# Optimization experiments

Hardware: AMD Instinct MI355X
Metric: run time of the kernel (lower is better)

## Reference

```python
import jax, jax.numpy as jnp
import numpy as np

H = 64          # hidden_size
L = 5           # num_layers
D_IN = 45       # input_size
D_LAT = 128     # latent dim
D_OUT = 4       # output classes


def _lstm_layer(x, W_ih, W_hh, b):
    """One LSTM layer, batch_first input x:[B,T,D]. PyTorch gate order i,f,g,o."""
    # Precompute input contribution for all timesteps: [B,T,4H]
    xg = jnp.einsum('btd,gd->btg', x, W_ih) + b
    xg = jnp.swapaxes(xg, 0, 1)  # [T,B,4H] for scan
    B = x.shape[0]
    h0 = jnp.zeros((B, H), x.dtype)
    c0 = jnp.zeros((B, H), x.dtype)

    def step(carry, xt):
        h, c = carry
        g = xt + h @ W_hh.T                      # [B,4H]
        i, f, gg, o = jnp.split(g, 4, axis=-1)
        c = jax.nn.sigmoid(f) * c + jax.nn.sigmoid(i) * jnp.tanh(gg)
        h = jax.nn.sigmoid(o) * jnp.tanh(c)
        return (h, c), h

    (_, _), hs = jax.lax.scan(step, (h0, c0), xg)  # hs: [T,B,H]
    return jnp.swapaxes(hs, 0, 1)                  # [B,T,H]


def setup_inputs() -> dict:
    key = jax.random.key(0)
    ks = jax.random.split(key, 12)
    s = 1.0 / np.sqrt(H)  # PyTorch LSTM init scale
    x = jax.random.normal(ks[0], (256, 2048, D_IN), jnp.float32)
    W_ih0 = jax.random.uniform(ks[1], (4 * H, D_IN), jnp.float32, -s, s)
    W_ih_rest = jax.random.uniform(ks[2], (L - 1, 4 * H, H), jnp.float32, -s, s)
    W_hh = jax.random.uniform(ks[3], (L, 4 * H, H), jnp.float32, -s, s)
    b_ih = jax.random.uniform(ks[4], (L, 4 * H), jnp.float32, -s, s)
    b_hh = jax.random.uniform(ks[5], (L, 4 * H), jnp.float32, -s, s)
    Wl = jax.random.normal(ks[6], (D_LAT, H), jnp.float32) * 0.05
    bl = jnp.zeros((D_LAT,), jnp.float32)
    Wo = jax.random.normal(ks[7], (D_OUT, D_LAT), jnp.float32) * 0.05
    bo = jnp.zeros((D_OUT,), jnp.float32)
    return dict(x=x, W_ih0=W_ih0, W_ih_rest=W_ih_rest, W_hh=W_hh,
                b_ih=b_ih, b_hh=b_hh, Wl=Wl, bl=bl, Wo=Wo, bo=bo)


def reference(x, W_ih0, W_ih_rest, W_hh, b_ih, b_hh, Wl, bl, Wo, bo):
    # 5-layer LSTM (eval mode: inter-layer dropout inactive)
    h = _lstm_layer(x, W_ih0, W_hh[0], b_ih[0] + b_hh[0])
    for l in range(1, L):
        h = _lstm_layer(h, W_ih_rest[l - 1], W_hh[l], b_ih[l] + b_hh[l])
    last = h[:, -1, :]                                  # [B,H]
    features = jax.nn.gelu(last @ Wl.T + bl, approximate=False)  # [B,128]
    out = jax.nn.relu(features @ Wo.T + bo)             # [B,4]
    return out, features
```

## Files before the change

### kernel.cpp

```cpp
#include <hip/hip_runtime.h>
#include <hip/hip_fp16.h>
#include <math.h>

#define NCH   1024
#define KMAX  1034
#define HID   64
typedef unsigned int uint;
typedef __attribute__((ext_vector_type(2))) _Float16 h2t;

__device__ __forceinline__ float sigmoid_(float x){ return 1.0f/(1.0f+__expf(-x)); }
__device__ __forceinline__ float tanh_(float x){ float e=__expf(2.0f*x); return 1.0f-2.0f/(e+1.0f); }

__device__ __forceinline__ float fdot2_(uint w, uint h, float acc){
#if __has_builtin(__builtin_amdgcn_fdot2)
    return __builtin_amdgcn_fdot2(__builtin_bit_cast(h2t,w), __builtin_bit_cast(h2t,h), acc, false);
#else
    __half2 wv = *reinterpret_cast<const __half2*>(&w);
    __half2 hv = *reinterpret_cast<const __half2*>(&h);
    float2 wf = __half22float2(wv), hf = __half22float2(hv);
    return fmaf(wf.x, hf.x, fmaf(wf.y, hf.y, acc));
#endif
}
__device__ __forceinline__ uint packh(float a, float b){
    uint ha = (uint)__half_as_ushort(__float2half(a));
    uint hb = (uint)__half_as_ushort(__float2half(b));
    return (hb<<16)|ha;
}
__device__ __forceinline__ uint4 pack8(const float* p){
    return make_uint4(packh(p[0],p[1]), packh(p[2],p[3]), packh(p[4],p[5]), packh(p[6],p[7]));
}

#define DOT4(A, W, H) do{ \
    A=fdot2_((W).x,(H).x,A); A=fdot2_((W).y,(H).y,A); \
    A=fdot2_((W).z,(H).z,A); A=fdot2_((W).w,(H).w,A); }while(0)

__global__ __attribute__((amdgpu_waves_per_eu(1,1))) __launch_bounds__(256)
void lstm_pipe4(const float* __restrict__ x,
                const float* __restrict__ W_ih0,
                const float* __restrict__ W_ih_rest,
                const float* __restrict__ W_hh,
                const float* __restrict__ b_ih,
                const float* __restrict__ b_hh,
                float* __restrict__ h_last)
{
    __shared__ float s_xg[2][5][2][256];
    __shared__ uint  s_wo [5][8][64][4];
    __shared__ uint  s_wih[10][8][64][4];
    __shared__ uint  s_hh[4][2][2][32];
    __shared__ uint  s_h16[5][32];
    __shared__ uint  s_x[2][2][24];

    const int tid  = threadIdx.x;
    const int wave = tid >> 6;
    const int lane = tid & 63;
    const int sm   = blockIdx.x;
    const float* x_s = x + (size_t)sm * 2048 * 45;
    float* hlast_g = h_last + (size_t)sm * HID;

    uint4 wU[48];
    float b0=0,b1=0,b2=0,b3=0,b4=0,b5=0,b6=0,b7=0,b8=0,b9=0;
    float cA=0.f, cB=0.f;

    if (wave == 0 || wave == 1){
#pragma unroll
        for (int li=0; li<2; ++li){
            const int L = wave*2 + li;
            const float* base = W_hh + (size_t)L*256*64;
#pragma unroll
            for (int d=0; d<8; ++d){
                wU[li*24 + 0*8 + d] = pack8(base + (size_t)(  0+lane)*64 + 8*d);
                wU[li*24 + 1*8 + d] = pack8(base + (size_t)( 64+lane)*64 + 8*d);
                wU[li*24 + 2*8 + d] = pack8(base + (size_t)(128+lane)*64 + 8*d);
                *(uint4*)&s_wo[L][d][lane][0] = pack8(base + (size_t)(192+lane)*64 + 8*d);
            }
            if (lane<32) s_h16[L][lane]=0u;
        }
#pragma unroll
        for (int g=0; g<2; ++g){
            const int row = wave*128 + g*64 + lane;
            const float* src = W_ih_rest + ((size_t)3*256 + row)*64;
            const int grp = 6 + wave*2 + g;
#pragma unroll
            for (int d=0; d<8; ++d)
                *(uint4*)&s_wih[grp][d][lane][0] = pack8(src + 8*d);
        }
        { int r0 = 4*256 + wave*128 + lane, r1 = r0 + 64;
          b0 = b_ih[r0]+b_hh[r0]; b1 = b_ih[r1]+b_hh[r1]; }
    } else if (wave == 2){
        const float* base = W_hh + (size_t)4*256*64;
#pragma unroll
        for (int d=0; d<8; ++d){
            wU[0*8+d] = pack8(base + (size_t)(  0+lane)*64 + 8*d);
            wU[1*8+d] = pack8(base + (size_t)( 64+lane)*64 + 8*d);
            wU[2*8+d] = pack8(base + (size_t)(128+lane)*64 + 8*d);
            *(uint4*)&s_wo[4][d][lane][0] = pack8(base + (size_t)(192+lane)*64 + 8*d);
        }
        if (lane<32) s_h16[4][lane]=0u;
#pragma unroll
        for (int g=0; g<4; ++g){
            const float* src = W_ih0 + (size_t)(g*64+lane)*45;
#pragma unroll
            for (int d=0; d<6; ++d){
                float e0=(8*d+0<45)?src[8*d+0]:0.f, e1=(8*d+1<45)?src[8*d+1]:0.f;
                float e2=(8*d+2<45)?src[8*d+2]:0.f, e3=(8*d+3<45)?src[8*d+3]:0.f;
                float e4=(8*d+4<45)?src[8*d+4]:0.f, e5=(8*d+5<45)?src[8*d+5]:0.f;
                float e6=(8*d+6<45)?src[8*d+6]:0.f, e7=(8*d+7<45)?src[8*d+7]:0.f;
                wU[24 + g*6 + d] = make_uint4(packh(e0,e1),packh(e2,e3),packh(e4,e5),packh(e6,e7));
            }
        }
        { int r;
          r=      lane; b0=b_ih[r]+b_hh[r];
          r=  64+lane;  b1=b_ih[r]+b_hh[r];
          r= 128+lane;  b2=b_ih[r]+b_hh[r];
          r= 192+lane;  b3=b_ih[r]+b_hh[r]; }
#pragma unroll
        for (int g=0; g<2; ++g){
            const int row = 128 + g*64 + lane;
            const float* src = W_ih_rest + ((size_t)1*256 + row)*64;
#pragma unroll
            for (int d=0; d<8; ++d)
                *(uint4*)&s_wih[g][d][lane][0] = pack8(src + 8*d);
        }
        { int r0=2*256+128+lane, r1=2*256+192+lane;
          b4=b_ih[r0]+b_hh[r0]; b5=b_ih[r1]+b_hh[r1]; }
        if (lane < 12){
            int bb=lane/6, t=(lane%6)/3, d=45+lane%3;
            ((__half*)&s_x[bb][t][0])[d]=__float2half(0.f);
        }
    } else {
#pragma unroll
        for (int g=0; g<6; ++g){
            const int ly  = (g<4) ? 1 : 2;
            const int row = (g<4) ? g*64+lane : (g-4)*64+lane;
            const float* src = W_ih_rest + ((size_t)(ly-1)*256 + row)*64;
#pragma unroll
            for (int d=0; d<8; ++d) wU[g*8+d] = pack8(src + 8*d);
        }
        { int r;
          r=1*256+  0+lane; b0=b_ih[r]+b_hh[r];
          r=1*256+ 64+lane; b1=b_ih[r]+b_hh[r];
          r=1*256+128+lane; b2=b_ih[r]+b_hh[r];
          r=1*256+192+lane; b3=b_ih[r]+b_hh[r];
          r=2*256+  0+lane; b4=b_ih[r]+b_hh[r];
          r=2*256+ 64+lane; b5=b_ih[r]+b_hh[r]; }
#pragma unroll
        for (int g=0; g<4; ++g){
            const float* src = W_ih_rest + ((size_t)2*256 + g*64+lane)*64;
#pragma unroll
            for (int d=0; d<8; ++d) *(uint4*)&s_wih[2+g][d][lane][0] = pack8(src + 8*d);
        }
        { int r;
          r=3*256+  0+lane; b6=b_ih[r]+b_hh[r];
          r=3*256+ 64+lane; b7=b_ih[r]+b_hh[r];
          r=3*256+128+lane; b8=b_ih[r]+b_hh[r];
          r=3*256+192+lane; b9=b_ih[r]+b_hh[r]; }
    }
    __syncthreads();

#define R_STEPN(L, WB, LASTF, T, C, CST) do{                                   \
    const int buf_ = (C)&1;                                                    \
    float xi_ = s_xg[buf_][L][T][      lane];                                  \
    float xf_ = s_xg[buf_][L][T][ 64 + lane];                                  \
    float xgg_= s_xg[buf_][L][T][128 + lane];                                  \
    float xo_ = s_xg[buf_][L][T][192 + lane];                                  \
    float ai0=0,ai1=0, af0=0,af1=0, ag0=0,ag1=0, ao0=0,ao1=0;                  \
    _Pragma("unroll")                                                          \
    for (int d_=0; d_<8; d_+=2){                                               \
        uint4 h0_ = *(const uint4*)&s_h16[L][4*d_];                            \
        uint4 h1_ = *(const uint4*)&s_h16[L][4*d_+4];                          \
        uint4 woA_ = *(const uint4*)&s_wo[L][d_  ][lane][0];                   \
        uint4 woB_ = *(const uint4*)&s_wo[L][d_+1][lane][0];                   \
        DOT4(ai0, wU[(WB)+d_],      h0_); DOT4(ai1, wU[(WB)+d_+1],    h1_);    \
        DOT4(af0, wU[(WB)+8+d_],    h0_); DOT4(af1, wU[(WB)+8+d_+1],  h1_);    \
        DOT4(ag0, wU[(WB)+16+d_],   h0_); DOT4(ag1, wU[(WB)+16+d_+1], h1_);    \
        DOT4(ao0, woA_,             h0_); DOT4(ao1, woB_,             h1_);    \
    }                                                                          \
    float I_=sigmoid_(xi_+(ai0+ai1)), F_=sigmoid_(xf_+(af0+af1));              \
    float G_=tanh_(xgg_+(ag0+ag1)),   O_=sigmoid_(xo_+(ao0+ao1));              \
    CST = fmaf(F_, CST, I_*G_);                                                \
    float h_ = O_*tanh_(CST);                                                  \
    __half hhi_=__float2half(h_);                                              \
    ((__half*)&s_h16[L][0])[lane]=hhi_;                                        \
    if (!(LASTF)){                                                             \
        ((__half*)&s_hh[(L)<4?(L):0][buf_][T][0])[lane]=hhi_;                  \
    } else if ((C)==NCH-1 && (T)==1){ hlast_g[lane]=h_; }                      \
}while(0)

#define G4T(DMAX, WEXPR, H0, H1, XD0, XD1, B0_,B1_,B2_,B3_) do{                \
    float a00=(B0_),a01=(B1_),a02=(B2_),a03=(B3_);                             \
    float a10=(B0_),a11=(B1_),a12=(B2_),a13=(B3_);                             \
    _Pragma("unroll")                                                          \
    for (int d_=0; d_<(DMAX); ++d_){                                           \
        uint4 w0_=WEXPR(0,d_), w1_=WEXPR(1,d_), w2_=WEXPR(2,d_), w3_=WEXPR(3,d_);\
        uint4 h0_=*(const uint4*)&(H0)[4*d_];                                  \
        uint4 h1_=*(const uint4*)&(H1)[4*d_];                                  \
        DOT4(a00,w0_,h0_); DOT4(a01,w1_,h0_); DOT4(a02,w2_,h0_); DOT4(a03,w3_,h0_);\
        DOT4(a10,w0_,h1_); DOT4(a11,w1_,h1_); DOT4(a12,w2_,h1_); DOT4(a13,w3_,h1_);\
    }                                                                          \
    (XD0)[      lane]=a00; (XD0)[ 64+lane]=a01;                                \
    (XD0)[128+lane]=a02;   (XD0)[192+lane]=a03;                                \
    (XD1)[      lane]=a10; (XD1)[ 64+lane]=a11;                                \
    (XD1)[128+lane]=a12;   (XD1)[192+lane]=a13;                                \
}while(0)

#define G2T(DMAX, WEXPR, H0, H1, XD0, XD1, ROWOFF, B0_,B1_) do{                \
    float a00=(B0_),a01=(B1_), a10=(B0_),a11=(B1_);                            \
    _Pragma("unroll")                                                          \
    for (int d_=0; d_<(DMAX); ++d_){                                           \
        uint4 wa_ = WEXPR(0,d_), wb_ = WEXPR(1,d_);                            \
        uint4 h0_=*(const uint4*)&(H0)[4*d_];                                  \
        uint4 h1_=*(const uint4*)&(H1)[4*d_];                                  \
        DOT4(a00,wa_,h0_); DOT4(a01,wb_,h0_);                                  \
        DOT4(a10,wa_,h1_); DOT4(a11,wb_,h1_);                                  \
    }                                                                          \
    (XD0)[(ROWOFF)+lane]=a00; (XD0)[(ROWOFF)+64+lane]=a01;                     \
    (XD1)[(ROWOFF)+lane]=a10; (XD1)[(ROWOFF)+64+lane]=a11;                     \
}while(0)

#define W_L1(g,d)  wU[(g)*8+(d)]
#define W_L2R(g,d) wU[32+(g)*8+(d)]
#define W_L0(g,d)  wU[24+(g)*6+(d)]
#define W_L2L(g,d) (*(const uint4*)&s_wih[(g)][d][lane][0])
#define W_L3(g,d)  (*(const uint4*)&s_wih[2+(g)][d][lane][0])
#define W_L4A(g,d) (*(const uint4*)&s_wih[6+(g)][d][lane][0])
#define W_L4B(g,d) (*(const uint4*)&s_wih[8+(g)][d][lane][0])

#define STAGE_X() do{                                                          \
    const int bufx = k & 1;                                                    \
    _Pragma("unroll")                                                          \
    for (int r=0; r<2; ++r){                                                   \
        const int i = lane + 64*r;                                             \
        if (i < 90){                                                           \
            float v = x_s[(size_t)k*90 + i];                                   \
            const int t = i/45, d = i - 45*t;                                  \
            ((__half*)&s_x[bufx][t][0])[d] = __float2half(v);                  \
        }                                                                      \
    }                                                                          \
}while(0)

#define BODY_W0(GUARDED) do{                                                   \
    const int c0=k-2, c1=k-4, cl=k-9;                                          \
    if (!(GUARDED) || (c0>=0 && c0<NCH)){                                      \
        R_STEPN(0,  0, 0, 0, c0, cA); }                                        \
    if (!(GUARDED) || (c1>=0 && c1<NCH)){                                      \
        R_STEPN(1, 24, 0, 0, c1, cB); }                                        \
    if (!(GUARDED) || (c0>=0 && c0<NCH)){                                      \
        R_STEPN(0,  0, 0, 1, c0, cA); }                                        \
    if (!(GUARDED) || (c1>=0 && c1<NCH)){                                      \
        R_STEPN(1, 24, 0, 1, c1, cB); }                                        \
    if (!(GUARDED) || (cl>=0 && cl<NCH)){                                      \
        const int bl=cl&1;                                                     \
        G2T(8, W_L4A, (&s_hh[3][bl][0][0]), (&s_hh[3][bl][1][0]),              \
            (&s_xg[bl][4][0][0]), (&s_xg[bl][4][1][0]), 0, b0,b1); }           \
}while(0)

#define BODY_W1(GUARDED) do{                                                   \
    const int c2=k-6, c3=k-8, cl=k-9;                                          \
    if (!(GUARDED) || (c2>=0 && c2<NCH)){                                      \
        R_STEPN(2,  0, 0, 0, c2, cA); }                                        \
    if (!(GUARDED) || (c3>=0 && c3<NCH)){                                      \
        R_STEPN(3, 24, 0, 0, c3, cB); }                                        \
    if (!(GUARDED) || (c2>=0 && c2<NCH)){                                      \
        R_STEPN(2,  0, 0, 1, c2, cA); }                                        \
    if (!(GUARDED) || (c3>=0 && c3<NCH)){                                      \
        R_STEPN(3, 24, 0, 1, c3, cB); }                                        \
    if (!(GUARDED) || (cl>=0 && cl<NCH)){                                      \
        const int bl=cl&1;                                                     \
        G2T(8, W_L4B, (&s_hh[3][bl][0][0]), (&s_hh[3][bl][1][0]),              \
            (&s_xg[bl][4][0][0]), (&s_xg[bl][4][1][0]), 128, b0,b1); }         \
}while(0)

#define BODY_W2(GUARDED) do{                                                   \
    if (!(GUARDED) || (k < NCH)) STAGE_X();                                    \
    const int c4=k-10, cg0=k-1, cg2=k-5;                                       \
    if (!(GUARDED) || (c4>=0 && c4<NCH)){                                      \
        R_STEPN(4, 0, 1, 0, c4, cA); }                                         \
    if (!(GUARDED) || (cg0>=0 && cg0<NCH)){                                    \
        const int bg=cg0&1;                                                    \
        G4T(6, W_L0, (&s_x[bg][0][0]), (&s_x[bg][1][0]),                       \
            (&s_xg[bg][0][0][0]), (&s_xg[bg][0][1][0]), b0,b1,b2,b3); }        \
    if (!(GUARDED) || (c4>=0 && c4<NCH)){                                      \
        R_STEPN(4, 0, 1, 1, c4, cA); }                                         \
    if (!(GUARDED) || (cg2>=0 && cg2<NCH)){                                    \
        const int bg=cg2&1;                                                    \
        G2T(8, W_L2L, (&s_hh[1][bg][0][0]), (&s_hh[1][bg][1][0]),              \
            (&s_xg[bg][2][0][0]), (&s_xg[bg][2][1][0]), 128, b4,b5); }         \
}while(0)

#define BODY_W3(GUARDED) do{                                                   \
    const int cg1=k-3, cg2=k-5, cg3=k-7;                                       \
    if (!(GUARDED) || (cg1>=0 && cg1<NCH)){                                    \
        const int bg=cg1&1;                                                    \
        G4T(8, W_L1, (&s_hh[0][bg][0][0]), (&s_hh[0][bg][1][0]),               \
            (&s_xg[bg][1][0][0]), (&s_xg[bg][1][1][0]), b0,b1,b2,b3); }        \
    if (!(GUARDED) || (cg2>=0 && cg2<NCH)){                                    \
        const int bg=cg2&1;                                                    \
        G2T(8, W_L2R, (&s_hh[1][bg][0][0]), (&s_hh[1][bg][1][0]),              \
            (&s_xg[bg][2][0][0]), (&s_xg[bg][2][1][0]), 0, b4,b5); }           \
    if (!(GUARDED) || (cg3>=0 && cg3<NCH)){                                    \
        const int bg=cg3&1;                                                    \
        G4T(8, W_L3, (&s_hh[2][bg][0][0]), (&s_hh[2][bg][1][0]),               \
            (&s_xg[bg][3][0][0]), (&s_xg[bg][3][1][0]), b6,b7,b8,b9); }        \
}while(0)

    for (int k=0; k<KMAX; ++k){
        if (k >= 10 && k < NCH){
            if      (wave == 0) BODY_W0(0);
            else if (wave == 1) BODY_W1(0);
            else if (wave == 2) BODY_W2(0);
            else                BODY_W3(0);
        } else {
            if      (wave == 0) BODY_W0(1);
            else if (wave == 1) BODY_W1(1);
            else if (wave == 2) BODY_W2(1);
            else                BODY_W3(1);
        }
        __syncthreads();
    }
}

__global__ __launch_bounds__(128)
void head_kernel(const float* __restrict__ h_last,
                 const float* __restrict__ Wl,
                 const float* __restrict__ bl,
                 const float* __restrict__ Wo,
                 const float* __restrict__ bo,
                 float* __restrict__ d_out)
{
    __shared__ float s_last[HID];
    __shared__ float s_feat[128];
    const int s = blockIdx.x;
    const int j = threadIdx.x;

    if (j < HID) s_last[j] = h_last[(size_t)s * HID + j];
    __syncthreads();

    float acc = bl[j];
#pragma unroll
    for (int k = 0; k < HID; ++k)
        acc = fmaf(s_last[k], Wl[j * HID + k], acc);
    float f = 0.5f * acc * (1.0f + erff(acc * 0.70710678118654752440f));
    d_out[256 * 4 + s * 128 + j] = f;
    s_feat[j] = f;
    __syncthreads();

    if (j < 4) {
        float a = bo[j];
#pragma unroll
        for (int k = 0; k < 128; ++k)
            a = fmaf(s_feat[k], Wo[j * 128 + k], a);
        d_out[s * 4 + j] = fmaxf(a, 0.0f);
    }
}

extern "C" void kernel_launch(void* const* d_in, const int* in_sizes, int n_in,
                              void* d_out, int out_size, void* d_ws, size_t ws_size,
                              hipStream_t stream)
{
    const float* x         = (const float*)d_in[0];
    const float* W_ih0     = (const float*)d_in[1];
    const float* W_ih_rest = (const float*)d_in[2];
    const float* W_hh      = (const float*)d_in[3];
    const float* b_ih      = (const float*)d_in[4];
    const float* b_hh      = (const float*)d_in[5];
    const float* Wl        = (const float*)d_in[6];
    const float* bl        = (const float*)d_in[7];
    const float* Wo        = (const float*)d_in[8];
    const float* bo        = (const float*)d_in[9];

    float* h_last = (float*)d_ws;

    lstm_pipe4<<<256, 256, 0, stream>>>(
        x, W_ih0, W_ih_rest, W_hh, b_ih, b_hh, h_last);
    head_kernel<<<256, 128, 0, stream>>>(h_last, Wl, bl, Wo, bo, (float*)d_out);
}
```

Baseline: 4.621 ms.

## Process four timesteps per pipeline chunk and store gate preactivations as fp16

Doubles the chunk size of the wavefront-pipelined LSTM from two to four timesteps, halving the number of chunk iterations and block-wide barriers. The input-projection buffers are switched to half precision so the larger chunk still fits in shared memory, and new one-gate, four-timestep projection helpers replace the two-timestep ones. This cuts synchronisation overhead per timestep, but adds fp16 rounding on the gate preactivations, which may hurt accuracy, and lengthens each wave's work per stage.

New measurement: 10.41 ms. +125.3%, slower.

```diff
diff --git a/kernel.cpp b/kernel.cpp
--- a/kernel.cpp
+++ b/kernel.cpp
@@ -2,8 +2,9 @@
 #include <hip/hip_fp16.h>
 #include <math.h>
 
-#define NCH   1024
-#define KMAX  1034
+#define CH    4
+#define NCH   512
+#define KMAX  522
 #define HID   64
 typedef unsigned int uint;
 typedef __attribute__((ext_vector_type(2))) _Float16 h2t;
@@ -43,12 +44,12 @@
                 const float* __restrict__ b_hh,
                 float* __restrict__ h_last)
 {
-    __shared__ float s_xg[2][5][2][256];
+    __shared__ __half s_xg[2][5][CH][256];
     __shared__ uint  s_wo [5][8][64][4];
     __shared__ uint  s_wih[10][8][64][4];
-    __shared__ uint  s_hh[4][2][2][32];
+    __shared__ uint  s_hh[4][2][CH][32];
     __shared__ uint  s_h16[5][32];
-    __shared__ uint  s_x[2][2][24];
+    __shared__ uint  s_x[2][CH][24];
 
     const int tid  = threadIdx.x;
     const int wave = tid >> 6;
@@ -123,8 +124,8 @@
         }
         { int r0=2*256+128+lane, r1=2*256+192+lane;
           b4=b_ih[r0]+b_hh[r0]; b5=b_ih[r1]+b_hh[r1]; }
-        if (lane < 12){
-            int bb=lane/6, t=(lane%6)/3, d=45+lane%3;
+        if (lane < 2*CH*3){
+            int bb=lane/(CH*3), rem=lane%(CH*3), t=rem/3, d=45+rem%3;
             ((__half*)&s_x[bb][t][0])[d]=__float2half(0.f);
         }
     } else {
@@ -159,10 +160,10 @@
 
 #define R_STEPN(L, WB, LASTF, T, C, CST) do{                                   \
     const int buf_ = (C)&1;                                                    \
-    float xi_ = s_xg[buf_][L][T][      lane];                                  \
-    float xf_ = s_xg[buf_][L][T][ 64 + lane];                                  \
-    float xgg_= s_xg[buf_][L][T][128 + lane];                                  \
-    float xo_ = s_xg[buf_][L][T][192 + lane];                                  \
+    float xi_ = __half2float(s_xg[buf_][L][T][      lane]);                    \
+    float xf_ = __half2float(s_xg[buf_][L][T][ 64 + lane]);                    \
+    float xgg_= __half2float(s_xg[buf_][L][T][128 + lane]);                    \
+    float xo_ = __half2float(s_xg[buf_][L][T][192 + lane]);                    \
     float ai0=0,ai1=0, af0=0,af1=0, ag0=0,ag1=0, ao0=0,ao1=0;                  \
     _Pragma("unroll")                                                          \
     for (int d_=0; d_<8; d_+=2){                                               \
@@ -183,7 +184,25 @@
     ((__half*)&s_h16[L][0])[lane]=hhi_;                                        \
     if (!(LASTF)){                                                             \
         ((__half*)&s_hh[(L)<4?(L):0][buf_][T][0])[lane]=hhi_;                  \
-    } else if ((C)==NCH-1 && (T)==1){ hlast_g[lane]=h_; }                      \
+    } else if ((C)==NCH-1 && (T)==CH-1){ hlast_g[lane]=h_; }                   \
+}while(0)
+
+#define G1Q(DMAX, WEXPR, HB, HSTR, XB, ROWOFF, B0_) do{                        \
+    float a0=(B0_),a1=(B0_),a2=(B0_),a3=(B0_);                                 \
+    _Pragma("unroll")                                                          \
+    for (int d_=0; d_<(DMAX); ++d_){                                           \
+        uint4 w_ = WEXPR(d_);                                                  \
+        uint4 h0_=*(const uint4*)&(HB)[0*(HSTR)+4*d_];                         \
+        uint4 h1_=*(const uint4*)&(HB)[1*(HSTR)+4*d_];                         \
+        uint4 h2_=*(const uint4*)&(HB)[2*(HSTR)+4*d_];                         \
+        uint4 h3_=*(const uint4*)&(HB)[3*(HSTR)+4*d_];                         \
+        DOT4(a0,w_,h0_); DOT4(a1,w_,h1_); DOT4(a2,w_,h2_); DOT4(a3,w_,h3_);    \
+    }                                                                          \
+    __half* xp_ = (__half*)(XB);                                               \
+    xp_[0*256+(ROWOFF)+lane]=__float2half(a0);                                 \
+    xp_[1*256+(ROWOFF)+lane]=__float2half(a1);                                 \
+    xp_[2*256+(ROWOFF)+lane]=__float2half(a2);                                 \
+    xp_[3*256+(ROWOFF)+lane]=__float2half(a3);                                 \
 }while(0)
 
 #define G4T(DMAX, WEXPR, H0, H1, XD0, XD1, B0_,B1_,B2_,B3_) do{                \
@@ -197,10 +216,12 @@
         DOT4(a00,w0_,h0_); DOT4(a01,w1_,h0_); DOT4(a02,w2_,h0_); DOT4(a03,w3_,h0_);\
         DOT4(a10,w0_,h1_); DOT4(a11,w1_,h1_); DOT4(a12,w2_,h1_); DOT4(a13,w3_,h1_);\
     }                                                                          \
-    (XD0)[      lane]=a00; (XD0)[ 64+lane]=a01;                                \
-    (XD0)[128+lane]=a02;   (XD0)[192+lane]=a03;                                \
-    (XD1)[      lane]=a10; (XD1)[ 64+lane]=a11;                                \
-    (XD1)[128+lane]=a12;   (XD1)[192+lane]=a13;                                \
+    __half* xp0_ = (__half*)(XD0);                                             \
+    __half* xp1_ = (__half*)(XD1);                                             \
+    xp0_[      lane]=__float2half(a00); xp0_[ 64+lane]=__float2half(a01);      \
+    xp0_[128+lane]=__float2half(a02);   xp0_[192+lane]=__float2half(a03);      \
+    xp1_[      lane]=__float2half(a10); xp1_[ 64+lane]=__float2half(a11);      \
+    xp1_[128+lane]=__float2half(a12);   xp1_[192+lane]=__float2half(a13);      \
 }while(0)
 
 #define G2T(DMAX, WEXPR, H0, H1, XD0, XD1, ROWOFF, B0_,B1_) do{                \
@@ -213,25 +234,33 @@
         DOT4(a00,wa_,h0_); DOT4(a01,wb_,h0_);                                  \
         DOT4(a10,wa_,h1_); DOT4(a11,wb_,h1_);                                  \
     }                                                                          \
-    (XD0)[(ROWOFF)+lane]=a00; (XD0)[(ROWOFF)+64+lane]=a01;                     \
-    (XD1)[(ROWOFF)+lane]=a10; (XD1)[(ROWOFF)+64+lane]=a11;                     \
+    __half* xp0_ = (__half*)(XD0);                                             \
+    __half* xp1_ = (__half*)(XD1);                                             \
+    xp0_[(ROWOFF)+lane]=__float2half(a00); xp0_[(ROWOFF)+64+lane]=__float2half(a01);\
+    xp1_[(ROWOFF)+lane]=__float2half(a10); xp1_[(ROWOFF)+64+lane]=__float2half(a11);\
 }while(0)
 
 #define W_L1(g,d)  wU[(g)*8+(d)]
 #define W_L2R(g,d) wU[32+(g)*8+(d)]
 #define W_L0(g,d)  wU[24+(g)*6+(d)]
-#define W_L2L(g,d) (*(const uint4*)&s_wih[(g)][d][lane][0])
-#define W_L3(g,d)  (*(const uint4*)&s_wih[2+(g)][d][lane][0])
-#define W_L4A(g,d) (*(const uint4*)&s_wih[6+(g)][d][lane][0])
-#define W_L4B(g,d) (*(const uint4*)&s_wih[8+(g)][d][lane][0])
+#define WL2_0(d) (*(const uint4*)&s_wih[0][d][lane][0])
+#define WL2_1(d) (*(const uint4*)&s_wih[1][d][lane][0])
+#define WL3_0(d) (*(const uint4*)&s_wih[2][d][lane][0])
+#define WL3_1(d) (*(const uint4*)&s_wih[3][d][lane][0])
+#define WL3_2(d) (*(const uint4*)&s_wih[4][d][lane][0])
+#define WL3_3(d) (*(const uint4*)&s_wih[5][d][lane][0])
+#define WL4_0(d) (*(const uint4*)&s_wih[6][d][lane][0])
+#define WL4_1(d) (*(const uint4*)&s_wih[7][d][lane][0])
+#define WL4_2(d) (*(const uint4*)&s_wih[8][d][lane][0])
+#define WL4_3(d) (*(const uint4*)&s_wih[9][d][lane][0])
 
 #define STAGE_X() do{                                                          \
     const int bufx = k & 1;                                                    \
     _Pragma("unroll")                                                          \
-    for (int r=0; r<2; ++r){                                                   \
+    for (int r=0; r<3; ++r){                                                   \
         const int i = lane + 64*r;                                             \
-        if (i < 90){                                                           \
-            float v = x_s[(size_t)k*90 + i];                                   \
+        if (i < CH*45){                                                        \
+            float v = x_s[(size_t)k*(CH*45) + i];                              \
             const int t = i/45, d = i - 45*t;                                  \
             ((__half*)&s_x[bufx][t][0])[d] = __float2half(v);                  \
         }                                                                      \
@@ -240,51 +269,51 @@
 
 #define BODY_W0(GUARDED) do{                                                   \
     const int c0=k-2, c1=k-4, cl=k-9;                                          \
-    if (!(GUARDED) || (c0>=0 && c0<NCH)){                                      \
-        R_STEPN(0,  0, 0, 0, c0, cA); }                                        \
-    if (!(GUARDED) || (c1>=0 && c1<NCH)){                                      \
-        R_STEPN(1, 24, 0, 0, c1, cB); }                                        \
-    if (!(GUARDED) || (c0>=0 && c0<NCH)){                                      \
-        R_STEPN(0,  0, 0, 1, c0, cA); }                                        \
-    if (!(GUARDED) || (c1>=0 && c1<NCH)){                                      \
-        R_STEPN(1, 24, 0, 1, c1, cB); }                                        \
+    _Pragma("unroll 1")                                                        \
+    for (int t=0; t<CH; ++t){                                                  \
+        if (!(GUARDED) || (c0>=0 && c0<NCH)){ R_STEPN(0,  0, 0, t, c0, cA); }  \
+        if (!(GUARDED) || (c1>=0 && c1<NCH)){ R_STEPN(1, 24, 0, t, c1, cB); }  \
+    }                                                                          \
     if (!(GUARDED) || (cl>=0 && cl<NCH)){                                      \
         const int bl=cl&1;                                                     \
-        G2T(8, W_L4A, (&s_hh[3][bl][0][0]), (&s_hh[3][bl][1][0]),              \
-            (&s_xg[bl][4][0][0]), (&s_xg[bl][4][1][0]), 0, b0,b1); }           \
+        G1Q(8, WL4_0, (&s_hh[3][bl][0][0]), 32, (&s_xg[bl][4][0][0]),  0, b0); \
+        G1Q(8, WL4_1, (&s_hh[3][bl][0][0]), 32, (&s_xg[bl][4][0][0]), 64, b1); \
+    }                                                                          \
 }while(0)
 
 #define BODY_W1(GUARDED) do{                                                   \
     const int c2=k-6, c3=k-8, cl=k-9;                                          \
-    if (!(GUARDED) || (c2>=0 && c2<NCH)){                                      \
-        R_STEPN(2,  0, 0, 0, c2, cA); }                                        \
-    if (!(GUARDED) || (c3>=0 && c3<NCH)){                                      \
-        R_STEPN(3, 24, 0, 0, c3, cB); }                                        \
-    if (!(GUARDED) || (c2>=0 && c2<NCH)){                                      \
-        R_STEPN(2,  0, 0, 1, c2, cA); }                                        \
-    if (!(GUARDED) || (c3>=0 && c3<NCH)){                                      \
-        R_STEPN(3, 24, 0, 1, c3, cB); }                                        \
+    _Pragma("unroll 1")                                                        \
+    for (int t=0; t<CH; ++t){                                                  \
+        if (!(GUARDED) || (c2>=0 && c2<NCH)){ R_STEPN(2,  0, 0, t, c2, cA); }  \
+        if (!(GUARDED) || (c3>=0 && c3<NCH)){ R_STEPN(3, 24, 0, t, c3, cB); }  \
+    }                                                                          \
     if (!(GUARDED) || (cl>=0 && cl<NCH)){                                      \
         const int bl=cl&1;                                                     \
-        G2T(8, W_L4B, (&s_hh[3][bl][0][0]), (&s_hh[3][bl][1][0]),              \
-            (&s_xg[bl][4][0][0]), (&s_xg[bl][4][1][0]), 128, b0,b1); }         \
+        G1Q(8, WL4_2, (&s_hh[3][bl][0][0]), 32, (&s_xg[bl][4][0][0]), 128, b0);\
+        G1Q(8, WL4_3, (&s_hh[3][bl][0][0]), 32, (&s_xg[bl][4][0][0]), 192, b1);\
+    }                                                                          \
 }while(0)
 
 #define BODY_W2(GUARDED) do{                                                   \
     if (!(GUARDED) || (k < NCH)) STAGE_X();                                    \
     const int c4=k-10, cg0=k-1, cg2=k-5;                                       \
-    if (!(GUARDED) || (c4>=0 && c4<NCH)){                                      \
-        R_STEPN(4, 0, 1, 0, c4, cA); }                                         \
+    _Pragma("unroll 1")                                                        \
+    for (int t=0; t<CH; ++t){                                                  \
+        if (!(GUARDED) || (c4>=0 && c4<NCH)){ R_STEPN(4, 0, 1, t, c4, cA); }   \
+    }                                                                          \
     if (!(GUARDED) || (cg0>=0 && cg0<NCH)){                                    \
         const int bg=cg0&1;                                                    \
         G4T(6, W_L0, (&s_x[bg][0][0]), (&s_x[bg][1][0]),                       \
-            (&s_xg[bg][0][0][0]), (&s_xg[bg][0][1][0]), b0,b1,b2,b3); }        \
-    if (!(GUARDED) || (c4>=0 && c4<NCH)){                                      \
-        R_STEPN(4, 0, 1, 1, c4, cA); }                                         \
+            (&s_xg[bg][0][0][0]), (&s_xg[bg][0][1][0]), b0,b1,b2,b3);          \
+        G4T(6, W_L0, (&s_x[bg][2][0]), (&s_x[bg][3][0]),                       \
+            (&s_xg[bg][0][2][0]), (&s_xg[bg][0][3][0]), b0,b1,b2,b3);          \
+    }                                                                          \
     if (!(GUARDED) || (cg2>=0 && cg2<NCH)){                                    \
         const int bg=cg2&1;                                                    \
-        G2T(8, W_L2L, (&s_hh[1][bg][0][0]), (&s_hh[1][bg][1][0]),              \
-            (&s_xg[bg][2][0][0]), (&s_xg[bg][2][1][0]), 128, b4,b5); }         \
+        G1Q(8, WL2_0, (&s_hh[1][bg][0][0]), 32, (&s_xg[bg][2][0][0]), 128, b4);\
+        G1Q(8, WL2_1, (&s_hh[1][bg][0][0]), 32, (&s_xg[bg][2][0][0]), 192, b5);\
+    }                                                                          \
 }while(0)
 
 #define BODY_W3(GUARDED) do{                                                   \
@@ -292,15 +321,24 @@
     if (!(GUARDED) || (cg1>=0 && cg1<NCH)){                                    \
         const int bg=cg1&1;                                                    \
         G4T(8, W_L1, (&s_hh[0][bg][0][0]), (&s_hh[0][bg][1][0]),               \
-            (&s_xg[bg][1][0][0]), (&s_xg[bg][1][1][0]), b0,b1,b2,b3); }        \
+            (&s_xg[bg][1][0][0]), (&s_xg[bg][1][1][0]), b0,b1,b2,b3);          \
+        G4T(8, W_L1, (&s_hh[0][bg][2][0]), (&s_hh[0][bg][3][0]),               \
+            (&s_xg[bg][1][2][0]), (&s_xg[bg][1][3][0]), b0,b1,b2,b3);          \
+    }                                                                          \
     if (!(GUARDED) || (cg2>=0 && cg2<NCH)){                                    \
         const int bg=cg2&1;                                                    \
         G2T(8, W_L2R, (&s_hh[1][bg][0][0]), (&s_hh[1][bg][1][0]),              \
-            (&s_xg[bg][2][0][0]), (&s_xg[bg][2][1][0]), 0, b4,b5); }           \
+            (&s_xg[bg][2][0][0]), (&s_xg[bg][2][1][0]), 0, b4,b5);             \
+        G2T(8, W_L2R, (&s_hh[1][bg][2][0]), (&s_hh[1][bg][3][0]),              \
+            (&s_xg[bg][2][2][0]), (&s_xg[bg][2][3][0]), 0, b4,b5);             \
+    }                                                                          \
     if (!(GUARDED) || (cg3>=0 && cg3<NCH)){                                    \
         const int bg=cg3&1;                                                    \
-        G4T(8, W_L3, (&s_hh[2][bg][0][0]), (&s_hh[2][bg][1][0]),               \
-            (&s_xg[bg][3][0][0]), (&s_xg[bg][3][1][0]), b6,b7,b8,b9); }        \
+        G1Q(8, WL3_0, (&s_hh[2][bg][0][0]), 32, (&s_xg[bg][3][0][0]),   0, b6);\
+        G1Q(8, WL3_1, (&s_hh[2][bg][0][0]), 32, (&s_xg[bg][3][0][0]),  64, b7);\
+        G1Q(8, WL3_2, (&s_hh[2][bg][0][0]), 32, (&s_xg[bg][3][0][0]), 128, b8);\
+        G1Q(8, WL3_3, (&s_hh[2][bg][0][0]), 32, (&s_xg[bg][3][0][0]), 192, b9);\
+    }                                                                          \
 }while(0)
 
     for (int k=0; k<KMAX; ++k){
```
